# Kernel tuning notes

Hardware: AMD Instinct MI355X
Metric: run time of the kernel (lower is better)

## Reference

```python
import jax, jax.numpy as jnp
import numpy as np

NUM_HEADS = 12
HEAD_DIM = 64
SO3_DIM = 30  # round(64*0.5)//3*3
ROPE_FREQ = 100.0


def _rope1d(t, p):
    # t: [B,H,N,Dh], p: [B,N]
    half = t.shape[-1] // 2
    inv = 1.0 / (ROPE_FREQ ** (jnp.arange(half, dtype=jnp.float32) / half))
    ang = p[:, None, :, None] * inv  # [B,1,N,half]
    cos = jnp.concatenate([jnp.cos(ang)] * 2, axis=-1)
    sin = jnp.concatenate([jnp.sin(ang)] * 2, axis=-1)
    t1, t2 = t[..., :half], t[..., half:]
    return t * cos + jnp.concatenate([-t2, t1], axis=-1) * sin


def _rope2d(x, pos):
    # x: [B,H,N,D], pos: [B,N,2] (y,x)
    Dh = x.shape[-1] // 2
    return jnp.concatenate([
        _rope1d(x[..., :Dh], pos[..., 0]),
        _rope1d(x[..., Dh:], pos[..., 1]),
    ], axis=-1)


def _so3prope(t, R, num_img):
    # t: [B,H,S,Nt,Dh], R: [B,S,3,3]; rotate first SO3_DIM channels of the
    # first num_img (image) tokens as 3-vectors; special tokens untouched.
    img, sp = t[..., :num_img, :], t[..., num_img:, :]
    B, H, S, Ni, D = img.shape
    v = img[..., :SO3_DIM].reshape(B, H, S, Ni, SO3_DIM // 3, 3)
    v = jnp.einsum('bsij,bhsnkj->bhsnki', R, v).reshape(B, H, S, Ni, SO3_DIM)
    img = jnp.concatenate([v, img[..., SO3_DIM:]], axis=-1)
    return jnp.concatenate([img, sp], axis=-2)


def setup_inputs() -> dict:
    key = jax.random.key(0)
    ks = jax.random.split(key, 6)
    B, HW, S, Nt, C = 1, 576, 4, 577, 768
    G = 24  # 24x24 patch grid
    q_tokens = jax.random.normal(ks[0], (B, HW, C), dtype=jnp.float32)
    t_tokens = jax.random.normal(ks[1], (B, S, Nt, C), dtype=jnp.float32)
    yy, xx = jnp.meshgrid(jnp.arange(G, dtype=jnp.float32), jnp.arange(G, dtype=jnp.float32), indexing='ij')
    pos2d = jnp.broadcast_to(jnp.stack([yy, xx], axis=-1).reshape(1, HW, 2), (B, HW, 2))
    # random proper rotations via QR
    A = jax.random.normal(ks[2], (B, S, 3, 3), dtype=jnp.float32)
    Q, _ = jnp.linalg.qr(A)
    poses = jnp.tile(jnp.eye(4, dtype=jnp.float32), (B, S, 1, 1))
    template_poses = poses.at[:, :, :3, :3].set(Q)
    W_qkv = jax.random.normal(ks[3], (C, 3 * C), dtype=jnp.float32) * 0.02
    b_qkv = jnp.zeros((3 * C,), dtype=jnp.float32)
    W_proj = jax.random.normal(ks[4], (C, C), dtype=jnp.float32) * 0.02
    b_proj = jnp.zeros((C,), dtype=jnp.float32)
    return {'q_tokens': q_tokens, 't_tokens': t_tokens, 'pos2d': pos2d,
            'template_poses': template_poses, 'W_qkv': W_qkv, 'b_qkv': b_qkv,
            'W_proj': W_proj, 'b_proj': b_proj}


def reference(q_tokens, t_tokens, pos2d, template_poses, W_qkv, b_qkv, W_proj, b_proj):
    B, HW, C = q_tokens.shape
    S, Nt = t_tokens.shape[1], t_tokens.shape[2]
    x = jnp.concatenate([q_tokens, t_tokens.reshape(B, S * Nt, C)], axis=1)  # [B,N,C]
    N = x.shape[1]
    qkv = (x @ W_qkv + b_qkv).reshape(B, N, 3, NUM_HEADS, HEAD_DIM)
    q = jnp.transpose(qkv[:, :, 0], (0, 2, 1, 3))  # [B,H,N,d]
    k = jnp.transpose(qkv[:, :, 1], (0, 2, 1, 3))
    v = jnp.transpose(qkv[:, :, 2], (0, 2, 1, 3))
    # RoPE2D on query-image tokens only
    q = jnp.concatenate([_rope2d(q[:, :, :HW], pos2d), q[:, :, HW:]], axis=2)
    k = jnp.concatenate([_rope2d(k[:, :, :HW], pos2d), k[:, :, HW:]], axis=2)
    # SO3Prope on template image tokens
    R = template_poses[:, :, :3, :3]
    q_t = _so3prope(q[:, :, HW:].reshape(B, NUM_HEADS, S, Nt, HEAD_DIM), R, HW)
    k_t = _so3prope(k[:, :, HW:].reshape(B, NUM_HEADS, S, Nt, HEAD_DIM), R, HW)
    q = jnp.concatenate([q[:, :, :HW], q_t.reshape(B, NUM_HEADS, S * Nt, HEAD_DIM)], axis=2)
    k = jnp.concatenate([k[:, :, :HW], k_t.reshape(B, NUM_HEADS, S * Nt, HEAD_DIM)], axis=2)
    # SDPA (no mask, no dropout at eval)
    scale = HEAD_DIM ** -0.5
    attn = jax.nn.softmax(jnp.einsum('bhnd,bhmd->bhnm', q, k) * scale, axis=-1)
    out = jnp.einsum('bhnm,bhmd->bhnd', attn, v)
    out = jnp.transpose(out, (0, 2, 1, 3)).reshape(B, N, C)
    out = out @ W_proj + b_proj
    return out[:, :HW, :], out[:, HW:, :].reshape(B, S, Nt, C)
```

## Files before the change

kernel.cpp:

```cpp
#include <hip/hip_runtime.h>
#include <hip/hip_bf16.h>
#include <math.h>

#define N_TOK 2884
#define HW_IMG 576
#define NT_TOK 577
#define CDIM 768
#define NH 12
#define HD 64
#define QKV_COLS 2304
#define NVP 2944
#define NQT 46

typedef float f32x4 __attribute__((ext_vector_type(4)));
typedef short bf16x8 __attribute__((ext_vector_type(8)));
typedef unsigned short u16;
typedef unsigned short u16x8 __attribute__((ext_vector_type(8)));
typedef unsigned short u16x4 __attribute__((ext_vector_type(4)));
typedef unsigned int u32x4 __attribute__((ext_vector_type(4)));

static __device__ __forceinline__ u16 f2bf(float f) {
    union { __hip_bfloat16 b; u16 u; } cv;
    cv.b = __float2bfloat16(f);
    return cv.u;
}
static __device__ __forceinline__ float bf2f(u16 h) {
    return __uint_as_float(((unsigned)h) << 16);
}
static __device__ __forceinline__ void split1(float f, u16& h, u16& l) {
    h = f2bf(f);
    l = f2bf(f - bf2f(h));
}

__global__ __launch_bounds__(256)
void conv_x(const float* __restrict__ q, const float* __restrict__ t,
            u16* __restrict__ Xhi, u16* __restrict__ Xlo)
{
    const int i = (blockIdx.x * 256 + threadIdx.x) * 4;
    const int SPLIT = HW_IMG * CDIM;
    const float4 v = (i < SPLIT) ? *(const float4*)(q + i) : *(const float4*)(t + (i - SPLIT));
    u16x4 h, l;
    u16 hh, ll;
    split1(v.x, hh, ll); h[0] = hh; l[0] = ll;
    split1(v.y, hh, ll); h[1] = hh; l[1] = ll;
    split1(v.z, hh, ll); h[2] = hh; l[2] = ll;
    split1(v.w, hh, ll); h[3] = hh; l[3] = ll;
    *(u16x4*)(Xhi + i) = h;
    *(u16x4*)(Xlo + i) = l;
}

__global__ __launch_bounds__(256)
void conv_wT(const float* __restrict__ W, int ncols,
             u16* __restrict__ Thi, u16* __restrict__ Tlo)
{
    __shared__ float T[64][65];
    const int k0 = blockIdx.x * 64;
    const int n0 = blockIdx.y * 64;
    const int tid = threadIdx.x;
    {
        const int kr = tid >> 2, nch = (tid & 3) << 4;
        const float* src = W + (size_t)(k0 + kr) * ncols + n0 + nch;
        #pragma unroll
        for (int c = 0; c < 4; ++c) {
            const float4 f = *(const float4*)(src + c * 4);
            T[kr][nch + c * 4 + 0] = f.x;
            T[kr][nch + c * 4 + 1] = f.y;
            T[kr][nch + c * 4 + 2] = f.z;
            T[kr][nch + c * 4 + 3] = f.w;
        }
    }
    __syncthreads();
    const int nr = tid >> 2, kch = (tid & 3) << 4;
    u16x8 h0, h1, l0v, l1v;
    #pragma unroll
    for (int j = 0; j < 8; ++j) { u16 hh, ll; split1(T[kch + j][nr], hh, ll); h0[j] = hh; l0v[j] = ll; }
    #pragma unroll
    for (int j = 0; j < 8; ++j) { u16 hh, ll; split1(T[kch + 8 + j][nr], hh, ll); h1[j] = hh; l1v[j] = ll; }
    const size_t dst = (size_t)(n0 + nr) * CDIM + k0 + kch;
    *(u16x8*)(Thi + dst) = h0;     *(u16x8*)(Thi + dst + 8) = h1;
    *(u16x8*)(Tlo + dst) = l0v;    *(u16x8*)(Tlo + dst + 8) = l1v;
}

__global__ __launch_bounds__(256)
void qkv_mfma(const u16* __restrict__ Xhi, const u16* __restrict__ Xlo,
              const u16* __restrict__ Whi, const u16* __restrict__ Wlo,
              const float* __restrict__ bqkv,
              const float* __restrict__ pos2d, const float* __restrict__ tposes,
              u16* __restrict__ Qhi, u16* __restrict__ Qlo,
              u16* __restrict__ Khi, u16* __restrict__ Klo,
              u16* __restrict__ Vthi, u16* __restrict__ Vtlo)
{
    __shared__ __align__(16) u16 Ah[64][64], Al[64][64], Bh[64][64], Bl[64][64];
    __shared__ float Ct[64][65];

    const int rb = blockIdx.x;
    const int cb = blockIdx.y;
    const int which = cb / NH;
    const int h = cb - which * NH;
    const int colbase = cb * 64;
    const int tid = threadIdx.x;
    const int w = tid >> 6, l = tid & 63;
    const int lr = l & 15, lg = l >> 4;

    const int srow = tid >> 2, sch = (tid & 3) << 4;
    int arow = rb * 64 + srow;
    if (arow >= N_TOK) arow = N_TOK - 1;
    const size_t abase = (size_t)arow * CDIM + sch;
    const size_t bbase = (size_t)(colbase + srow) * CDIM + sch;

    f32x4 acc[4];
    #pragma unroll
    for (int i = 0; i < 4; ++i) acc[i] = (f32x4){0.f, 0.f, 0.f, 0.f};

    const int sw = (srow & 7) << 3;
    const int swf = (lr & 7) << 3;

    for (int k0 = 0; k0 < CDIM; k0 += 64) {
        const u16x8 a0h = *(const u16x8*)(Xhi + abase + k0);
        const u16x8 a1h = *(const u16x8*)(Xhi + abase + k0 + 8);
        const u16x8 a0l = *(const u16x8*)(Xlo + abase + k0);
        const u16x8 a1l = *(const u16x8*)(Xlo + abase + k0 + 8);
        const u16x8 b0h = *(const u16x8*)(Whi + bbase + k0);
        const u16x8 b1h = *(const u16x8*)(Whi + bbase + k0 + 8);
        const u16x8 b0l = *(const u16x8*)(Wlo + bbase + k0);
        const u16x8 b1l = *(const u16x8*)(Wlo + bbase + k0 + 8);
        __syncthreads();
        *(u16x8*)&Ah[srow][(sch + 0) ^ sw] = a0h;
        *(u16x8*)&Ah[srow][(sch + 8) ^ sw] = a1h;
        *(u16x8*)&Al[srow][(sch + 0) ^ sw] = a0l;
        *(u16x8*)&Al[srow][(sch + 8) ^ sw] = a1l;
        *(u16x8*)&Bh[srow][(sch + 0) ^ sw] = b0h;
        *(u16x8*)&Bh[srow][(sch + 8) ^ sw] = b1h;
        *(u16x8*)&Bl[srow][(sch + 0) ^ sw] = b0l;
        *(u16x8*)&Bl[srow][(sch + 8) ^ sw] = b1l;
        __syncthreads();
        #pragma unroll
        for (int ks = 0; ks < 2; ++ks) {
            const int koff = (ks * 32 + lg * 8) ^ swf;
            const bf16x8 ah_ = *(const bf16x8*)&Ah[w * 16 + lr][koff];
            const bf16x8 al_ = *(const bf16x8*)&Al[w * 16 + lr][koff];
            #pragma unroll
            for (int cbk = 0; cbk < 4; ++cbk) {
                const bf16x8 bh_ = *(const bf16x8*)&Bh[cbk * 16 + lr][koff];
                const bf16x8 bl_ = *(const bf16x8*)&Bl[cbk * 16 + lr][koff];
                acc[cbk] = __builtin_amdgcn_mfma_f32_16x16x32_bf16(ah_, bh_, acc[cbk], 0, 0, 0);
                acc[cbk] = __builtin_amdgcn_mfma_f32_16x16x32_bf16(ah_, bl_, acc[cbk], 0, 0, 0);
                acc[cbk] = __builtin_amdgcn_mfma_f32_16x16x32_bf16(al_, bh_, acc[cbk], 0, 0, 0);
            }
        }
    }

    #pragma unroll
    for (int cbk = 0; cbk < 4; ++cbk)
        #pragma unroll
        for (int r = 0; r < 4; ++r)
            Ct[w * 16 + lg * 4 + r][cbk * 16 + lr] = acc[cbk][r] + bqkv[colbase + cbk * 16 + lr];
    __syncthreads();

    if (which < 2) {
        const int er = tid >> 2;
        const int eu = tid & 3;
        const int n = rb * 64 + er;
        if (n < N_TOK) {
            float outv[16];
            const bool is_img = (n < HW_IMG);
            int ts = 0, tj = 0;
            if (!is_img) { const int m = n - HW_IMG; ts = m / NT_TOK; tj = m - ts * NT_TOK; }

            if (is_img) {
                const float p = (eu < 2) ? pos2d[2 * n] : pos2d[2 * n + 1];
                const bool lowhalf = ((eu & 1) == 0);
                #pragma unroll
                for (int dd = 0; dd < 16; ++dd) {
                    const int d = (eu << 4) + dd;
                    float sv, cv;
                    sincosf(p * expf((float)dd * -0.28782313662425574f), &sv, &cv);
                    const float rot = lowhalf ? -Ct[er][d + 16] : Ct[er][d - 16];
                    outv[dd] = Ct[er][d] * cv + rot * sv;
                }
            } else if (tj < HW_IMG) {
                #pragma unroll
                for (int dd = 0; dd < 16; ++dd) {
                    const int d = (eu << 4) + dd;
                    float val = Ct[er][d];
                    if (d < 30) {
                        const int g = d / 3;
                        const float* R = tposes + ts * 16 + (d - g * 3) * 4;
                        val = R[0] * Ct[er][g * 3] + R[1] * Ct[er][g * 3 + 1] + R[2] * Ct[er][g * 3 + 2];
                    }
                    outv[dd] = val;
                }
            } else {
                #pragma unroll
                for (int dd = 0; dd < 16; ++dd) outv[dd] = Ct[er][(eu << 4) + dd];
            }

            const float scale = (which == 0) ? 0.125f : 1.0f;
            u16x8 h0, h1, l0v, l1v;
            #pragma unroll
            for (int j = 0; j < 8; ++j) { u16 hh, ll; split1(outv[j] * scale, hh, ll); h0[j] = hh; l0v[j] = ll; }
            #pragma unroll
            for (int j = 0; j < 8; ++j) { u16 hh, ll; split1(outv[8 + j] * scale, hh, ll); h1[j] = hh; l1v[j] = ll; }
            u16* dh = (which == 0 ? Qhi : Khi) + ((size_t)h * N_TOK + n) * HD + (eu << 4);
            u16* dl = (which == 0 ? Qlo : Klo) + ((size_t)h * N_TOK + n) * HD + (eu << 4);
            *(u16x8*)dh = h0;  *(u16x8*)(dh + 8) = h1;
            *(u16x8*)dl = l0v; *(u16x8*)(dl + 8) = l1v;
        }
    } else {
        const int vd_ = tid >> 2, vch = (tid & 3) << 4;
        const int tokbase = rb * 64 + vch;
        u16 th[16], tl[16];
        #pragma unroll
        for (int j = 0; j < 16; ++j) { u16 hh, ll; split1(Ct[vch + j][vd_], hh, ll); th[j] = hh; tl[j] = ll; }
        u16* dh = Vthi + (size_t)(h * HD + vd_) * NVP + tokbase;
        u16* dl = Vtlo + (size_t)(h * HD + vd_) * NVP + tokbase;
        if (tokbase + 16 <= N_TOK) {
            *(u16x8*)dh = *(u16x8*)&th[0];  *(u16x8*)(dh + 8) = *(u16x8*)&th[8];
            *(u16x8*)dl = *(u16x8*)&tl[0];  *(u16x8*)(dl + 8) = *(u16x8*)&tl[8];
        } else {
            #pragma unroll
            for (int j = 0; j < 16; ++j)
                if (tokbase + j < N_TOK) { dh[j] = th[j]; dl[j] = tl[j]; }
        }
    }
}

__global__ __launch_bounds__(256, 3)
void attn_shard(const u16* __restrict__ Qhi, const u16* __restrict__ Qlo,
                const u16* __restrict__ Khi, const u16* __restrict__ Klo,
                const u16* __restrict__ Vthi, const u16* __restrict__ Vtlo,
                float* __restrict__ Pacc, float2* __restrict__ PmL,
                int TS, int SPLITS)
{
    __shared__ __align__(16) u16 Kh_s[64][64], Kl_s[64][64], Vh_s[64][64], Vl_s[64][64];
    __shared__ __align__(16) unsigned int P2[64][64];

    int qb, head, sh;
    {
        const int flat = blockIdx.x + NQT * (blockIdx.y + NH * blockIdx.z);
        if (SPLITS == 4) {
            const int grp = flat & 7;
            const int rest = flat >> 3;
            qb = rest % NQT;
            const int hs = grp + 8 * (rest / NQT);
            head = hs % NH;
            sh = hs / NH;
        } else {
            qb = blockIdx.x; head = blockIdx.y; sh = blockIdx.z;
        }
    }
    const int tid = threadIdx.x;
    const int w = tid >> 6, l = tid & 63;
    const int lr = l & 15, lg = l >> 4;

    const int kt_begin = sh * TS;
    const int kt_end = min(NQT, kt_begin + TS);

    bf16x8 qh_[2], ql_[2];
    {
        int row = qb * 64 + w * 16 + lr;
        if (row >= N_TOK) row = N_TOK - 1;
        const u16* qph = Qhi + ((size_t)head * N_TOK + row) * HD;
        const u16* qpl = Qlo + ((size_t)head * N_TOK + row) * HD;
        #pragma unroll
        for (int ks = 0; ks < 2; ++ks) {
            qh_[ks] = *(const bf16x8*)(qph + ks * 32 + lg * 8);
            ql_[ks] = *(const bf16x8*)(qpl + ks * 32 + lg * 8);
        }
    }

    float m0[4] = {-1e30f, -1e30f, -1e30f, -1e30f};
    float l0[4] = {0.f, 0.f, 0.f, 0.f};
    f32x4 acc[4];
    #pragma unroll
    for (int db = 0; db < 4; ++db) acc[db] = (f32x4){0.f, 0.f, 0.f, 0.f};

    const int skey = tid >> 2, sch = (tid & 3) << 4;
    const int vd_ = tid >> 2, vch = (tid & 3) << 4;
    const int swk = (skey & 7) << 3;
    const int swv = (vd_ & 7) << 3;
    const int swf = (lr & 7) << 3;
    const int swa = (lr & 7) << 2;
    const u16* KhH = Khi + (size_t)head * N_TOK * HD;
    const u16* KlH = Klo + (size_t)head * N_TOK * HD;
    const size_t vrowbase = (size_t)(head * HD + vd_) * NVP;

    u16x8 rk0h, rk1h, rk0l, rk1l, rv0h, rv1h, rv0l, rv1l;
    auto LOADT = [&](int kt) {
        const int kbase = kt << 6;
        int krow = kbase + skey;
        if (krow >= N_TOK) krow = N_TOK - 1;
        const u16* kph = KhH + (size_t)krow * HD + sch;
        const u16* kpl = KlH + (size_t)krow * HD + sch;
        rk0h = *(const u16x8*)kph;  rk1h = *(const u16x8*)(kph + 8);
        rk0l = *(const u16x8*)kpl;  rk1l = *(const u16x8*)(kpl + 8);
        const u16* vph = Vthi + vrowbase + kbase + vch;
        const u16* vpl = Vtlo + vrowbase + kbase + vch;
        rv0h = *(const u16x8*)vph;  rv1h = *(const u16x8*)(vph + 8);
        rv0l = *(const u16x8*)vpl;  rv1l = *(const u16x8*)(vpl + 8);
    };
    LOADT(kt_begin);

    for (int kt = kt_begin; kt < kt_end; ++kt) {
        const int kbase = kt << 6;

        __syncthreads();
        *(u16x8*)&Kh_s[skey][(sch + 0) ^ swk] = rk0h;
        *(u16x8*)&Kh_s[skey][(sch + 8) ^ swk] = rk1h;
        *(u16x8*)&Kl_s[skey][(sch + 0) ^ swk] = rk0l;
        *(u16x8*)&Kl_s[skey][(sch + 8) ^ swk] = rk1l;
        *(u16x8*)&Vh_s[vd_][(vch + 0) ^ swv] = rv0h;
        *(u16x8*)&Vh_s[vd_][(vch + 8) ^ swv] = rv1h;
        *(u16x8*)&Vl_s[vd_][(vch + 0) ^ swv] = rv0l;
        *(u16x8*)&Vl_s[vd_][(vch + 8) ^ swv] = rv1l;
        if (kt + 1 < kt_end) LOADT(kt + 1);
        __syncthreads();

        f32x4 s[4];
        __builtin_amdgcn_s_setprio(1);
        #pragma unroll
        for (int kb = 0; kb < 4; ++kb) {
            s[kb] = (f32x4){0.f, 0.f, 0.f, 0.f};
            const int key = kb * 16 + lr;
            #pragma unroll
            for (int ks = 0; ks < 2; ++ks) {
                const int koff = (ks * 32 + lg * 8) ^ swf;
                const bf16x8 bh = *(const bf16x8*)&Kh_s[key][koff];
                const bf16x8 bl = *(const bf16x8*)&Kl_s[key][koff];
                s[kb] = __builtin_amdgcn_mfma_f32_16x16x32_bf16(qh_[ks], bh, s[kb], 0, 0, 0);
                s[kb] = __builtin_amdgcn_mfma_f32_16x16x32_bf16(qh_[ks], bl, s[kb], 0, 0, 0);
                s[kb] = __builtin_amdgcn_mfma_f32_16x16x32_bf16(ql_[ks], bh, s[kb], 0, 0, 0);
            }
        }
        __builtin_amdgcn_s_setprio(0);

        if (kbase + 64 > N_TOK) {
            #pragma unroll
            for (int kb = 0; kb < 4; ++kb)
                if (kbase + kb * 16 + lr >= N_TOK) {
                    #pragma unroll
                    for (int r = 0; r < 4; ++r) s[kb][r] = -1e30f;
                }
        }

        float mt[4], al[4];
        #pragma unroll
        for (int r = 0; r < 4; ++r)
            mt[r] = fmaxf(fmaxf(s[0][r], s[1][r]), fmaxf(s[2][r], s[3][r]));
        #pragma unroll
        for (int r = 0; r < 4; ++r) {
            mt[r] = fmaxf(mt[r], __shfl_xor(mt[r], 1));
            mt[r] = fmaxf(mt[r], __shfl_xor(mt[r], 2));
            mt[r] = fmaxf(mt[r], __shfl_xor(mt[r], 4));
            mt[r] = fmaxf(mt[r], __shfl_xor(mt[r], 8));
        }
        #pragma unroll
        for (int r = 0; r < 4; ++r) {
            const float mn = fmaxf(m0[r], mt[r]);
            al[r] = __expf(m0[r] - mn);
            m0[r] = mn;
        }
        #pragma unroll
        for (int kb = 0; kb < 4; ++kb)
            #pragma unroll
            for (int r = 0; r < 4; ++r)
                s[kb][r] = __expf(s[kb][r] - m0[r]);
        #pragma unroll
        for (int r = 0; r < 4; ++r)
            l0[r] = l0[r] * al[r] + (s[0][r] + s[1][r] + s[2][r] + s[3][r]);
        #pragma unroll
        for (int db = 0; db < 4; ++db)
            #pragma unroll
            for (int r = 0; r < 4; ++r) acc[db][r] *= al[r];

        #pragma unroll
        for (int r = 0; r < 4; ++r) {
            const int rw = w * 16 + lg * 4 + r;
            const int swp = (rw & 7) << 2;
            #pragma unroll
            for (int kb = 0; kb < 4; ++kb) {
                const float p = s[kb][r];
                u16 ph, pl;
                split1(p, ph, pl);
                P2[rw][(kb * 16 + lr) ^ swp] = (unsigned)ph | ((unsigned)pl << 16);
            }
        }

        const int arow = w * 16 + lr;
        #pragma unroll
        for (int ks = 0; ks < 2; ++ks) {
            const int kb8 = ks * 32 + lg * 8;
            const u32x4 pa = *(const u32x4*)&P2[arow][(kb8 + 0) ^ swa];
            const u32x4 pb = *(const u32x4*)&P2[arow][(kb8 + 4) ^ swa];
            bf16x8 ph, pl;
            #pragma unroll
            for (int e = 0; e < 4; ++e) {
                ph[e]     = (short)(pa[e] & 0xffffu);
                pl[e]     = (short)(pa[e] >> 16);
                ph[4 + e] = (short)(pb[e] & 0xffffu);
                pl[4 + e] = (short)(pb[e] >> 16);
            }
            __builtin_amdgcn_s_setprio(1);
            #pragma unroll
            for (int db = 0; db < 4; ++db) {
                const int vr = db * 16 + lr;
                const int koff = kb8 ^ swf;
                const bf16x8 vh = *(const bf16x8*)&Vh_s[vr][koff];
                const bf16x8 vl = *(const bf16x8*)&Vl_s[vr][koff];
                acc[db] = __builtin_amdgcn_mfma_f32_16x16x32_bf16(ph, vh, acc[db], 0, 0, 0);
                acc[db] = __builtin_amdgcn_mfma_f32_16x16x32_bf16(ph, vl, acc[db], 0, 0, 0);
                acc[db] = __builtin_amdgcn_mfma_f32_16x16x32_bf16(pl, vh, acc[db], 0, 0, 0);
            }
            __builtin_amdgcn_s_setprio(0);
        }
    }

    #pragma unroll
    for (int r = 0; r < 4; ++r) {
        l0[r] += __shfl_xor(l0[r], 1);
        l0[r] += __shfl_xor(l0[r], 2);
        l0[r] += __shfl_xor(l0[r], 4);
        l0[r] += __shfl_xor(l0[r], 8);
    }
    const size_t pb = (((size_t)sh * NH + head) * NQT + qb) << 6;
    float* pout = Pacc + (pb << 6);
    #pragma unroll
    for (int r = 0; r < 4; ++r) {
        const int lrow = w * 16 + lg * 4 + r;
        #pragma unroll
        for (int db = 0; db < 4; ++db)
            pout[(size_t)lrow * 64 + db * 16 + lr] = acc[db][r];
        if (lr == 0)
            PmL[pb + lrow] = make_float2(m0[r], l0[r]);
    }
}

__global__ __launch_bounds__(256)
void attn_combine(const float* __restrict__ Pacc, const float2* __restrict__ PmL,
                  u16* __restrict__ Ohi, u16* __restrict__ Olo, int SPLITS)
{
    const int qb = blockIdx.x, h = blockIdx.y;
    const int tid = threadIdx.x;
    const int er = tid >> 2, eu = tid & 3;
    const int row = qb * 64 + er;
    if (row >= N_TOK) return;

    float ms[4], ls[4];
    float m = -1e30f;
    for (int s = 0; s < SPLITS; ++s) {
        const float2 p = PmL[((((size_t)s * NH + h) * NQT + qb) << 6) + er];
        ms[s] = p.x; ls[s] = p.y;
        m = fmaxf(m, p.x);
    }
    float L = 0.f, Ws[4];
    for (int s = 0; s < SPLITS; ++s) { Ws[s] = __expf(ms[s] - m); L += ls[s] * Ws[s]; }
    const float inv = 1.f / L;

    float o[16];
    #pragma unroll
    for (int j = 0; j < 16; ++j) o[j] = 0.f;
    for (int s = 0; s < SPLITS; ++s) {
        const float* src = Pacc + ((((((size_t)s * NH + h) * NQT + qb) << 6) + er) << 6) + (eu << 4);
        const float wgt = Ws[s];
        #pragma unroll
        for (int c = 0; c < 4; ++c) {
            const float4 f = *(const float4*)(src + c * 4);
            o[c * 4 + 0] += wgt * f.x;
            o[c * 4 + 1] += wgt * f.y;
            o[c * 4 + 2] += wgt * f.z;
            o[c * 4 + 3] += wgt * f.w;
        }
    }
    u16x8 h0, h1, l0v, l1v;
    #pragma unroll
    for (int j = 0; j < 8; ++j) { u16 hh, ll; split1(o[j] * inv, hh, ll); h0[j] = hh; l0v[j] = ll; }
    #pragma unroll
    for (int j = 0; j < 8; ++j) { u16 hh, ll; split1(o[8 + j] * inv, hh, ll); h1[j] = hh; l1v[j] = ll; }
    u16* dh = Ohi + (size_t)row * CDIM + h * HD + (eu << 4);
    u16* dl = Olo + (size_t)row * CDIM + h * HD + (eu << 4);
    *(u16x8*)dh = h0;  *(u16x8*)(dh + 8) = h1;
    *(u16x8*)dl = l0v; *(u16x8*)(dl + 8) = l1v;
}

__global__ __launch_bounds__(256)
void proj_mfma(const u16* __restrict__ Ahi, const u16* __restrict__ Alo,
               const u16* __restrict__ Whi, const u16* __restrict__ Wlo,
               const float* __restrict__ bp, float* __restrict__ out)
{
    __shared__ __align__(16) u16 Ah[64][64], Al[64][64], Bh[64][64], Bl[64][64];

    const int rb = blockIdx.x;
    const int colbase = blockIdx.y * 64;
    const int tid = threadIdx.x;
    const int w = tid >> 6, l = tid & 63;
    const int lr = l & 15, lg = l >> 4;

    const int srow = tid >> 2, sch = (tid & 3) << 4;
    int arow = rb * 64 + srow;
    if (arow >= N_TOK) arow = N_TOK - 1;
    const size_t abase = (size_t)arow * CDIM + sch;
    const size_t bbase = (size_t)(colbase + srow) * CDIM + sch;

    f32x4 acc[4];
    #pragma unroll
    for (int i = 0; i < 4; ++i) acc[i] = (f32x4){0.f, 0.f, 0.f, 0.f};

    const int sw = (srow & 7) << 3;
    const int swf = (lr & 7) << 3;

    for (int k0 = 0; k0 < CDIM; k0 += 64) {
        const u16x8 a0h = *(const u16x8*)(Ahi + abase + k0);
        const u16x8 a1h = *(const u16x8*)(Ahi + abase + k0 + 8);
        const u16x8 a0l = *(const u16x8*)(Alo + abase + k0);
        const u16x8 a1l = *(const u16x8*)(Alo + abase + k0 + 8);
        const u16x8 b0h = *(const u16x8*)(Whi + bbase + k0);
        const u16x8 b1h = *(const u16x8*)(Whi + bbase + k0 + 8);
        const u16x8 b0l = *(const u16x8*)(Wlo + bbase + k0);
        const u16x8 b1l = *(const u16x8*)(Wlo + bbase + k0 + 8);
        __syncthreads();
        *(u16x8*)&Ah[srow][(sch + 0) ^ sw] = a0h;
        *(u16x8*)&Ah[srow][(sch + 8) ^ sw] = a1h;
        *(u16x8*)&Al[srow][(sch + 0) ^ sw] = a0l;
        *(u16x8*)&Al[srow][(sch + 8) ^ sw] = a1l;
        *(u16x8*)&Bh[srow][(sch + 0) ^ sw] = b0h;
        *(u16x8*)&Bh[srow][(sch + 8) ^ sw] = b1h;
        *(u16x8*)&Bl[srow][(sch + 0) ^ sw] = b0l;
        *(u16x8*)&Bl[srow][(sch + 8) ^ sw] = b1l;
        __syncthreads();
        #pragma unroll
        for (int ks = 0; ks < 2; ++ks) {
            const int koff = (ks * 32 + lg * 8) ^ swf;
            const bf16x8 ah_ = *(const bf16x8*)&Ah[w * 16 + lr][koff];
            const bf16x8 al_ = *(const bf16x8*)&Al[w * 16 + lr][koff];
            #pragma unroll
            for (int cbk = 0; cbk < 4; ++cbk) {
                const bf16x8 bh_ = *(const bf16x8*)&Bh[cbk * 16 + lr][koff];
                const bf16x8 bl_ = *(const bf16x8*)&Bl[cbk * 16 + lr][koff];
                acc[cbk] = __builtin_amdgcn_mfma_f32_16x16x32_bf16(ah_, bh_, acc[cbk], 0, 0, 0);
                acc[cbk] = __builtin_amdgcn_mfma_f32_16x16x32_bf16(ah_, bl_, acc[cbk], 0, 0, 0);
                acc[cbk] = __builtin_amdgcn_mfma_f32_16x16x32_bf16(al_, bh_, acc[cbk], 0, 0, 0);
            }
        }
    }

    #pragma unroll
    for (int cbk = 0; cbk < 4; ++cbk) {
        const float bb = bp[colbase + cbk * 16 + lr];
        #pragma unroll
        for (int r = 0; r < 4; ++r) {
            const int row = rb * 64 + w * 16 + lg * 4 + r;
            if (row < N_TOK)
                out[(size_t)row * CDIM + colbase + cbk * 16 + lr] = acc[cbk][r] + bb;
        }
    }
}

extern "C" void kernel_launch(void* const* d_in, const int* in_sizes, int n_in,
                              void* d_out, int out_size, void* d_ws, size_t ws_size,
                              hipStream_t stream)
{
    const float* q_tokens = (const float*)d_in[0];
    const float* t_tokens = (const float*)d_in[1];
    const float* pos2d    = (const float*)d_in[2];
    const float* tposes   = (const float*)d_in[3];
    const float* Wqkv     = (const float*)d_in[4];
    const float* bqkv     = (const float*)d_in[5];
    const float* Wproj    = (const float*)d_in[6];
    const float* bproj    = (const float*)d_in[7];
    float* out = (float*)d_out;

    const size_t PQ = (size_t)NH * N_TOK * HD;
    const size_t PV_ = (size_t)NH * HD * NVP;
    const size_t PX = (size_t)N_TOK * CDIM;
    const size_t PW = (size_t)QKV_COLS * CDIM;

    u16* base = (u16*)d_ws;
    u16* Qhi  = base;
    u16* Qlo  = Qhi + PQ;
    u16* Khi  = Qlo + PQ;
    u16* Klo  = Khi + PQ;
    u16* Vthi = Klo + PQ;
    u16* Vtlo = Vthi + PV_;
    u16* XOhi = Vtlo + PV_;
    u16* XOlo = XOhi + PX;
    u16* WThi = XOlo + PX;
    u16* WTlo = WThi + PW;
    u16* planes_end = WTlo + PW;

    const size_t planes_bytes = (size_t)(planes_end - base) * sizeof(u16);
    const size_t accElems = (size_t)NH * NQT * 64 * 64;
    const size_t mlElems  = (size_t)NH * NQT * 64;
    const size_t per_shard = accElems * 4 + mlElems * 8;

    int SPLITS = 1;
    for (int cand = 4; cand >= 2; --cand) {
        if (planes_bytes + (size_t)cand * per_shard <= ws_size) { SPLITS = cand; break; }
    }
    float* Pacc = (float*)((char*)d_ws + planes_bytes);
    float2* PmL = (float2*)(Pacc + (size_t)SPLITS * accElems);
    const int TS = (NQT + SPLITS - 1) / SPLITS;

    conv_x<<<dim3((N_TOK * CDIM / 4 + 255) / 256), 256, 0, stream>>>(q_tokens, t_tokens, XOhi, XOlo);
    conv_wT<<<dim3(CDIM / 64, QKV_COLS / 64), 256, 0, stream>>>(Wqkv, QKV_COLS, WThi, WTlo);
    hipMemsetAsync(Vthi, 0, 2 * PV_ * sizeof(u16), stream);

    dim3 g1((N_TOK + 63) / 64, 36);
    qkv_mfma<<<g1, 256, 0, stream>>>(XOhi, XOlo, WThi, WTlo, bqkv, pos2d, tposes,
                                     Qhi, Qlo, Khi, Klo, Vthi, Vtlo);

    conv_wT<<<dim3(CDIM / 64, CDIM / 64), 256, 0, stream>>>(Wproj, CDIM, WThi, WTlo);

    dim3 g2(NQT, NH, SPLITS);
    attn_shard<<<g2, 256, 0, stream>>>(Qhi, Qlo, Khi, Klo, Vthi, Vtlo, Pacc, PmL, TS, SPLITS);

    dim3 g2b(NQT, NH);
    attn_combine<<<g2b, 256, 0, stream>>>(Pacc, PmL, XOhi, XOlo, SPLITS);

    dim3 g3((N_TOK + 63) / 64, CDIM / 64);
    proj_mfma<<<g3, 256, 0, stream>>>(XOhi, XOlo, WThi, WTlo, bproj, out);
}
```

Baseline: 220.8 us.

## Switch PV product to fp16 single-P MFMA and enlarge QKV GEMM row tile

The attention PV product now stores P as a single fp16 value instead of a bf16 hi/lo pair. V is split into fp16 hi/lo, so each step needs two f16 MFMAs instead of three bf16 ones, and the P LDS buffer is halved. The QKV GEMM tile grows from 64 to 128 rows per block, with shared memory unioned between the staging tiles and the output tile, to get more reuse of the weight tiles. Launch bounds are raised to allow more resident blocks. Rounding P to fp16 (11-bit mantissa) gives up some accuracy compared with the split-bf16 scheme.

```diff
diff --git a/kernel.cpp b/kernel.cpp
--- a/kernel.cpp
+++ b/kernel.cpp
@@ -1,5 +1,6 @@
 #include <hip/hip_runtime.h>
 #include <hip/hip_bf16.h>
+#include <hip/hip_fp16.h>
 #include <math.h>
 
 #define N_TOK 2884
@@ -14,10 +15,10 @@
 
 typedef float f32x4 __attribute__((ext_vector_type(4)));
 typedef short bf16x8 __attribute__((ext_vector_type(8)));
+typedef _Float16 f16x8 __attribute__((ext_vector_type(8)));
 typedef unsigned short u16;
 typedef unsigned short u16x8 __attribute__((ext_vector_type(8)));
 typedef unsigned short u16x4 __attribute__((ext_vector_type(4)));
-typedef unsigned int u32x4 __attribute__((ext_vector_type(4)));
 
 static __device__ __forceinline__ u16 f2bf(float f) {
     union { __hip_bfloat16 b; u16 u; } cv;
@@ -30,6 +31,14 @@
 static __device__ __forceinline__ void split1(float f, u16& h, u16& l) {
     h = f2bf(f);
     l = f2bf(f - bf2f(h));
+}
+static __device__ __forceinline__ void split1h(float f, u16& h, u16& l) {
+    const __half hh = __float2half(f);
+    h = __half_as_ushort(hh);
+    l = __half_as_ushort(__float2half(f - __half2float(hh)));
+}
+static __device__ __forceinline__ f16x8 as_f16x8(u16x8 u) {
+    union { u16x8 u; f16x8 h; } c; c.u = u; return c.h;
 }
 
 __global__ __launch_bounds__(256)
@@ -81,7 +90,7 @@
     *(u16x8*)(Tlo + dst) = l0v;    *(u16x8*)(Tlo + dst + 8) = l1v;
 }
 
-__global__ __launch_bounds__(256)
+__global__ __launch_bounds__(256, 3)
 void qkv_mfma(const u16* __restrict__ Xhi, const u16* __restrict__ Xlo,
               const u16* __restrict__ Whi, const u16* __restrict__ Wlo,
               const float* __restrict__ bqkv,
@@ -90,8 +99,12 @@
               u16* __restrict__ Khi, u16* __restrict__ Klo,
               u16* __restrict__ Vthi, u16* __restrict__ Vtlo)
 {
-    __shared__ __align__(16) u16 Ah[64][64], Al[64][64], Bh[64][64], Bl[64][64];
-    __shared__ float Ct[64][65];
+    __shared__ __align__(16) char smem[49152];
+    u16 (*Ah)[64] = (u16(*)[64])(smem);
+    u16 (*Al)[64] = (u16(*)[64])(smem + 16384);
+    u16 (*Bh)[64] = (u16(*)[64])(smem + 32768);
+    u16 (*Bl)[64] = (u16(*)[64])(smem + 40960);
+    float (*Ct)[65] = (float(*)[65])(smem);
 
     const int rb = blockIdx.x;
     const int cb = blockIdx.y;
@@ -102,138 +115,168 @@
     const int w = tid >> 6, l = tid & 63;
     const int lr = l & 15, lg = l >> 4;
 
-    const int srow = tid >> 2, sch = (tid & 3) << 4;
-    int arow = rb * 64 + srow;
+    const int sa_r = tid >> 1;
+    const int sa_c = (tid & 1) << 5;
+    int arow = rb * 128 + sa_r;
     if (arow >= N_TOK) arow = N_TOK - 1;
-    const size_t abase = (size_t)arow * CDIM + sch;
-    const size_t bbase = (size_t)(colbase + srow) * CDIM + sch;
-
-    f32x4 acc[4];
-    #pragma unroll
-    for (int i = 0; i < 4; ++i) acc[i] = (f32x4){0.f, 0.f, 0.f, 0.f};
-
-    const int sw = (srow & 7) << 3;
+    const size_t abase = (size_t)arow * CDIM + sa_c;
+    const int swa_ = (sa_r & 7) << 3;
+    const int sb_r = tid >> 2;
+    const int sb_c = (tid & 3) << 4;
+    const size_t bbase = (size_t)(colbase + sb_r) * CDIM + sb_c;
+    const int swb_ = (sb_r & 7) << 3;
+
     const int swf = (lr & 7) << 3;
 
+    f32x4 acc[2][4];
+    #pragma unroll
+    for (int rf = 0; rf < 2; ++rf)
+        #pragma unroll
+        for (int i = 0; i < 4; ++i) acc[rf][i] = (f32x4){0.f, 0.f, 0.f, 0.f};
+
     for (int k0 = 0; k0 < CDIM; k0 += 64) {
-        const u16x8 a0h = *(const u16x8*)(Xhi + abase + k0);
-        const u16x8 a1h = *(const u16x8*)(Xhi + abase + k0 + 8);
-        const u16x8 a0l = *(const u16x8*)(Xlo + abase + k0);
-        const u16x8 a1l = *(const u16x8*)(Xlo + abase + k0 + 8);
-        const u16x8 b0h = *(const u16x8*)(Whi + bbase + k0);
-        const u16x8 b1h = *(const u16x8*)(Whi + bbase + k0 + 8);
-        const u16x8 b0l = *(const u16x8*)(Wlo + bbase + k0);
-        const u16x8 b1l = *(const u16x8*)(Wlo + bbase + k0 + 8);
+        u16x8 a_h[4], a_l[4], b_h[2], b_l[2];
+        #pragma unroll
+        for (int c = 0; c < 4; ++c) {
+            a_h[c] = *(const u16x8*)(Xhi + abase + k0 + c * 8);
+            a_l[c] = *(const u16x8*)(Xlo + abase + k0 + c * 8);
+        }
+        #pragma unroll
+        for (int c = 0; c < 2; ++c) {
+            b_h[c] = *(const u16x8*)(Whi + bbase + k0 + c * 8);
+            b_l[c] = *(const u16x8*)(Wlo + bbase + k0 + c * 8);
+        }
         __syncthreads();
-        *(u16x8*)&Ah[srow][(sch + 0) ^ sw] = a0h;
-        *(u16x8*)&Ah[srow][(sch + 8) ^ sw] = a1h;
-        *(u16x8*)&Al[srow][(sch + 0) ^ sw] = a0l;
-        *(u16x8*)&Al[srow][(sch + 8) ^ sw] = a1l;
-        *(u16x8*)&Bh[srow][(sch + 0) ^ sw] = b0h;
-        *(u16x8*)&Bh[srow][(sch + 8) ^ sw] = b1h;
-        *(u16x8*)&Bl[srow][(sch + 0) ^ sw] = b0l;
-        *(u16x8*)&Bl[srow][(sch + 8) ^ sw] = b1l;
+        #pragma unroll
+        for (int c = 0; c < 4; ++c) {
+            *(u16x8*)&Ah[sa_r][(sa_c + c * 8) ^ swa_] = a_h[c];
+            *(u16x8*)&Al[sa_r][(sa_c + c * 8) ^ swa_] = a_l[c];
+        }
+        #pragma unroll
+        for (int c = 0; c < 2; ++c) {
+            *(u16x8*)&Bh[sb_r][(sb_c + c * 8) ^ swb_] = b_h[c];
+            *(u16x8*)&Bl[sb_r][(sb_c + c * 8) ^ swb_] = b_l[c];
+        }
         __syncthreads();
         #pragma unroll
         for (int ks = 0; ks < 2; ++ks) {
             const int koff = (ks * 32 + lg * 8) ^ swf;
-            const bf16x8 ah_ = *(const bf16x8*)&Ah[w * 16 + lr][koff];
-            const bf16x8 al_ = *(const bf16x8*)&Al[w * 16 + lr][koff];
+            const bf16x8 ah0 = *(const bf16x8*)&Ah[w * 32 + lr][koff];
+            const bf16x8 al0 = *(const bf16x8*)&Al[w * 32 + lr][koff];
+            const bf16x8 ah1 = *(const bf16x8*)&Ah[w * 32 + 16 + lr][koff];
+            const bf16x8 al1 = *(const bf16x8*)&Al[w * 32 + 16 + lr][koff];
             #pragma unroll
             for (int cbk = 0; cbk < 4; ++cbk) {
                 const bf16x8 bh_ = *(const bf16x8*)&Bh[cbk * 16 + lr][koff];
                 const bf16x8 bl_ = *(const bf16x8*)&Bl[cbk * 16 + lr][koff];
-                acc[cbk] = __builtin_amdgcn_mfma_f32_16x16x32_bf16(ah_, bh_, acc[cbk], 0, 0, 0);
-                acc[cbk] = __builtin_amdgcn_mfma_f32_16x16x32_bf16(ah_, bl_, acc[cbk], 0, 0, 0);
-                acc[cbk] = __builtin_amdgcn_mfma_f32_16x16x32_bf16(al_, bh_, acc[cbk], 0, 0, 0);
+                acc[0][cbk] = __builtin_amdgcn_mfma_f32_16x16x32_bf16(ah0, bh_, acc[0][cbk], 0, 0, 0);
+                acc[0][cbk] = __builtin_amdgcn_mfma_f32_16x16x32_bf16(ah0, bl_, acc[0][cbk], 0, 0, 0);
+                acc[0][cbk] = __builtin_amdgcn_mfma_f32_16x16x32_bf16(al0, bh_, acc[0][cbk], 0, 0, 0);
+                acc[1][cbk] = __builtin_amdgcn_mfma_f32_16x16x32_bf16(ah1, bh_, acc[1][cbk], 0, 0, 0);
+                acc[1][cbk] = __builtin_amdgcn_mfma_f32_16x16x32_bf16(ah1, bl_, acc[1][cbk], 0, 0, 0);
+                acc[1][cbk] = __builtin_amdgcn_mfma_f32_16x16x32_bf16(al1, bh_, acc[1][cbk], 0, 0, 0);
             }
         }
     }
 
-    #pragma unroll
-    for (int cbk = 0; cbk < 4; ++cbk)
-        #pragma unroll
-        for (int r = 0; r < 4; ++r)
-            Ct[w * 16 + lg * 4 + r][cbk * 16 + lr] = acc[cbk][r] + bqkv[colbase + cbk * 16 + lr];
     __syncthreads();
+    #pragma unroll
+    for (int rf = 0; rf < 2; ++rf)
+        #pragma unroll
+        for (int cbk = 0; cbk < 4; ++cbk)
+            #pragma unroll
+            for (int r = 0; r < 4; ++r)
+                Ct[w * 32 + rf * 16 + lg * 4 + r][cbk * 16 + lr] =
+                    acc[rf][cbk][r] + bqkv[colbase + cbk * 16 + lr];
+    __syncthreads();
 
     if (which < 2) {
-        const int er = tid >> 2;
-        const int eu = tid & 3;
-        const int n = rb * 64 + er;
-        if (n < N_TOK) {
-            float outv[16];
-            const bool is_img = (n < HW_IMG);
-            int ts = 0, tj = 0;
-            if (!is_img) { const int m = n - HW_IMG; ts = m / NT_TOK; tj = m - ts * NT_TOK; }
-
-            if (is_img) {
-                const float p = (eu < 2) ? pos2d[2 * n] : pos2d[2 * n + 1];
-                const bool lowhalf = ((eu & 1) == 0);
+        #pragma unroll
+        for (int it = 0; it < 2; ++it) {
+            const int item = it * 256 + tid;
+            const int er = item >> 2;
+            const int eu = item & 3;
+            const int n = rb * 128 + er;
+            if (n < N_TOK) {
+                float outv[16];
+                const bool is_img = (n < HW_IMG);
+                int ts = 0, tj = 0;
+                if (!is_img) { const int m = n - HW_IMG; ts = m / NT_TOK; tj = m - ts * NT_TOK; }
+
+                if (is_img) {
+                    const float p = (eu < 2) ? pos2d[2 * n] : pos2d[2 * n + 1];
+                    const bool lowhalf = ((eu & 1) == 0);
+                    #pragma unroll
+                    for (int dd = 0; dd < 16; ++dd) {
+                        const int d = (eu << 4) + dd;
+                        float sv, cv;
+                        sincosf(p * expf((float)dd * -0.28782313662425574f), &sv, &cv);
+                        const float rot = lowhalf ? -Ct[er][d + 16] : Ct[er][d - 16];
+                        outv[dd] = Ct[er][d] * cv + rot * sv;
+                    }
+                } else if (tj < HW_IMG) {
+                    #pragma unroll
+                    for (int dd = 0; dd < 16; ++dd) {
+                        const int d = (eu << 4) + dd;
+                        float val = Ct[er][d];
+                        if (d < 30) {
+                            const int g = d / 3;
+                            const float* R = tposes + ts * 16 + (d - g * 3) * 4;
+                            val = R[0] * Ct[er][g * 3] + R[1] * Ct[er][g * 3 + 1] + R[2] * Ct[er][g * 3 + 2];
+                        }
+                        outv[dd] = val;
+                    }
+                } else {
+                    #pragma unroll
+                    for (int dd = 0; dd < 16; ++dd) outv[dd] = Ct[er][(eu << 4) + dd];
+                }
+
+                const float scale = (which == 0) ? 0.125f : 1.0f;
+                u16x8 h0, h1, l0v, l1v;
                 #pragma unroll
-                for (int dd = 0; dd < 16; ++dd) {
-                    const int d = (eu << 4) + dd;
-                    float sv, cv;
-                    sincosf(p * expf((float)dd * -0.28782313662425574f), &sv, &cv);
-                    const float rot = lowhalf ? -Ct[er][d + 16] : Ct[er][d - 16];
-                    outv[dd] = Ct[er][d] * cv + rot * sv;
-                }
-            } else if (tj < HW_IMG) {
+                for (int j = 0; j < 8; ++j) { u16 hh, ll; split1(outv[j] * scale, hh, ll); h0[j] = hh; l0v[j] = ll; }
                 #pragma unroll
-                for (int dd = 0; dd < 16; ++dd) {
-                    const int d = (eu << 4) + dd;
-                    float val = Ct[er][d];
-                    if (d < 30) {
-                        const int g = d / 3;
-                        const float* R = tposes + ts * 16 + (d - g * 3) * 4;
-                        val = R[0] * Ct[er][g * 3] + R[1] * Ct[er][g * 3 + 1] + R[2] * Ct[er][g * 3 + 2];
-                    }
-                    outv[dd] = val;
-                }
+                for (int j = 0; j < 8; ++j) { u16 hh, ll; split1(outv[8 + j] * scale, hh, ll); h1[j] = hh; l1v[j] = ll; }
+                u16* dh = (which == 0 ? Qhi : Khi) + ((size_t)h * N_TOK + n) * HD + (eu << 4);
+                u16* dl = (which == 0 ? Qlo : Klo) + ((size_t)h * N_TOK + n) * HD + (eu << 4);
+                *(u16x8*)dh = h0;  *(u16x8*)(dh + 8) = h1;
+                *(u16x8*)dl = l0v; *(u16x8*)(dl + 8) = l1v;
+            }
+        }
+    } else {
+        #pragma unroll
+        for (int it = 0; it < 2; ++it) {
+            const int item = it * 256 + tid;
+            const int vd_ = item >> 3;
+            const int vch = (item & 7) << 4;
+            const int tokbase = rb * 128 + vch;
+            u16 th[16], tl[16];
+            #pragma unroll
+            for (int j = 0; j < 16; ++j) { u16 hh, ll; split1h(Ct[vch + j][vd_], hh, ll); th[j] = hh; tl[j] = ll; }
+            u16* dh = Vthi + (size_t)(h * HD + vd_) * NVP + tokbase;
+            u16* dl = Vtlo + (size_t)(h * HD + vd_) * NVP + tokbase;
+            if (tokbase + 16 <= N_TOK) {
+                *(u16x8*)dh = *(u16x8*)&th[0];  *(u16x8*)(dh + 8) = *(u16x8*)&th[8];
+                *(u16x8*)dl = *(u16x8*)&tl[0];  *(u16x8*)(dl + 8) = *(u16x8*)&tl[8];
             } else {
                 #pragma unroll
-                for (int dd = 0; dd < 16; ++dd) outv[dd] = Ct[er][(eu << 4) + dd];
+                for (int j = 0; j < 16; ++j)
+                    if (tokbase + j < N_TOK) { dh[j] = th[j]; dl[j] = tl[j]; }
             }
-
-            const float scale = (which == 0) ? 0.125f : 1.0f;
-            u16x8 h0, h1, l0v, l1v;
-            #pragma unroll
-            for (int j = 0; j < 8; ++j) { u16 hh, ll; split1(outv[j] * scale, hh, ll); h0[j] = hh; l0v[j] = ll; }
-            #pragma unroll
-            for (int j = 0; j < 8; ++j) { u16 hh, ll; split1(outv[8 + j] * scale, hh, ll); h1[j] = hh; l1v[j] = ll; }
-            u16* dh = (which == 0 ? Qhi : Khi) + ((size_t)h * N_TOK + n) * HD + (eu << 4);
-            u16* dl = (which == 0 ? Qlo : Klo) + ((size_t)h * N_TOK + n) * HD + (eu << 4);
-            *(u16x8*)dh = h0;  *(u16x8*)(dh + 8) = h1;
-            *(u16x8*)dl = l0v; *(u16x8*)(dl + 8) = l1v;
-        }
-    } else {
-        const int vd_ = tid >> 2, vch = (tid & 3) << 4;
-        const int tokbase = rb * 64 + vch;
-        u16 th[16], tl[16];
-        #pragma unroll
-        for (int j = 0; j < 16; ++j) { u16 hh, ll; split1(Ct[vch + j][vd_], hh, ll); th[j] = hh; tl[j] = ll; }
-        u16* dh = Vthi + (size_t)(h * HD + vd_) * NVP + tokbase;
-        u16* dl = Vtlo + (size_t)(h * HD + vd_) * NVP + tokbase;
-        if (tokbase + 16 <= N_TOK) {
-            *(u16x8*)dh = *(u16x8*)&th[0];  *(u16x8*)(dh + 8) = *(u16x8*)&th[8];
-            *(u16x8*)dl = *(u16x8*)&tl[0];  *(u16x8*)(dl + 8) = *(u16x8*)&tl[8];
-        } else {
-            #pragma unroll
-            for (int j = 0; j < 16; ++j)
-                if (tokbase + j < N_TOK) { dh[j] = th[j]; dl[j] = tl[j]; }
-        }
-    }
-}
-
-__global__ __launch_bounds__(256, 3)
+        }
+    }
+}
+
+__global__ __launch_bounds__(256, 4)
 void attn_shard(const u16* __restrict__ Qhi, const u16* __restrict__ Qlo,
                 const u16* __restrict__ Khi, const u16* __restrict__ Klo,
                 const u16* __restrict__ Vthi, const u16* __restrict__ Vtlo,
                 float* __restrict__ Pacc, float2* __restrict__ PmL,
                 int TS, int SPLITS)
 {
-    __shared__ __align__(16) u16 Kh_s[64][64], Kl_s[64][64], Vh_s[64][64], Vl_s[64][64];
-    __shared__ __align__(16) unsigned int P2[64][64];
+    __shared__ __align__(16) u16 Kh_s[64][64], Kl_s[64][64];
+    __shared__ __align__(16) u16 Vh_s[64][64], Vl_s[64][64];
+    __shared__ __align__(16) u16 P2[64][64];
 
     int qb, head, sh;
     {
@@ -280,7 +323,6 @@
     const int swk = (skey & 7) << 3;
     const int swv = (vd_ & 7) << 3;
     const int swf = (lr & 7) << 3;
-    const int swa = (lr & 7) << 2;
     const u16* KhH = Khi + (size_t)head * N_TOK * HD;
     const u16* KlH = Klo + (size_t)head * N_TOK * HD;
     const size_t vrowbase = (size_t)(head * HD + vd_) * NVP;
@@ -376,40 +418,27 @@
         #pragma unroll
         for (int r = 0; r < 4; ++r) {
             const int rw = w * 16 + lg * 4 + r;
-            const int swp = (rw & 7) << 2;
-            #pragma unroll
-            for (int kb = 0; kb < 4; ++kb) {
-                const float p = s[kb][r];
-                u16 ph, pl;
-                split1(p, ph, pl);
-                P2[rw][(kb * 16 + lr) ^ swp] = (unsigned)ph | ((unsigned)pl << 16);
-            }
+            const int swp = (rw & 7) << 3;
+            #pragma unroll
+            for (int kb = 0; kb < 4; ++kb)
+                P2[rw][(kb * 16 + lr) ^ swp] = __half_as_ushort(__float2half(s[kb][r]));
         }
 
         const int arow = w * 16 + lr;
+        const int swpa = (arow & 7) << 3;
         #pragma unroll
         for (int ks = 0; ks < 2; ++ks) {
             const int kb8 = ks * 32 + lg * 8;
-            const u32x4 pa = *(const u32x4*)&P2[arow][(kb8 + 0) ^ swa];
-            const u32x4 pb = *(const u32x4*)&P2[arow][(kb8 + 4) ^ swa];
-            bf16x8 ph, pl;
-            #pragma unroll
-            for (int e = 0; e < 4; ++e) {
-                ph[e]     = (short)(pa[e] & 0xffffu);
-                pl[e]     = (short)(pa[e] >> 16);
-                ph[4 + e] = (short)(pb[e] & 0xffffu);
-                pl[4 + e] = (short)(pb[e] >> 16);
-            }
+            const f16x8 pa = as_f16x8(*(const u16x8*)&P2[arow][kb8 ^ swpa]);
             __builtin_amdgcn_s_setprio(1);
             #pragma unroll
             for (int db = 0; db < 4; ++db) {
                 const int vr = db * 16 + lr;
                 const int koff = kb8 ^ swf;
-                const bf16x8 vh = *(const bf16x8*)&Vh_s[vr][koff];
-                const bf16x8 vl = *(const bf16x8*)&Vl_s[vr][koff];
-                acc[db] = __builtin_amdgcn_mfma_f32_16x16x32_bf16(ph, vh, acc[db], 0, 0, 0);
-                acc[db] = __builtin_amdgcn_mfma_f32_16x16x32_bf16(ph, vl, acc[db], 0, 0, 0);
-                acc[db] = __builtin_amdgcn_mfma_f32_16x16x32_bf16(pl, vh, acc[db], 0, 0, 0);
+                const f16x8 vh = as_f16x8(*(const u16x8*)&Vh_s[vr][koff]);
+                const f16x8 vl = as_f16x8(*(const u16x8*)&Vl_s[vr][koff]);
+                acc[db] = __builtin_amdgcn_mfma_f32_16x16x32_f16(pa, vh, acc[db], 0, 0, 0);
+                acc[db] = __builtin_amdgcn_mfma_f32_16x16x32_f16(pa, vl, acc[db], 0, 0, 0);
             }
             __builtin_amdgcn_s_setprio(0);
         }
@@ -604,7 +633,7 @@
     conv_wT<<<dim3(CDIM / 64, QKV_COLS / 64), 256, 0, stream>>>(Wqkv, QKV_COLS, WThi, WTlo);
     hipMemsetAsync(Vthi, 0, 2 * PV_ * sizeof(u16), stream);
 
-    dim3 g1((N_TOK + 63) / 64, 36);
+    dim3 g1((N_TOK + 127) / 128, 36);
     qkv_mfma<<<g1, 256, 0, stream>>>(XOhi, XOlo, WThi, WTlo, bqkv, pos2d, tposes,
                                      Qhi, Qlo, Khi, Klo, Vthi, Vtlo);
 
```

New measurement: 255.7 us. 1.16x slower.
